# Kernel optimization log

Hardware: AMD Instinct MI355X
Metric: run time of the kernel (lower is better)

The kernel has to match this reference:

```python
import jax, jax.numpy as jnp
import numpy as np

IMAGE_MAX_DIM = 1024.0
POOL_H, POOL_W = 7, 7
LEVEL_THRESH = 48.0


def crop_and_resize(image, boxes, box_idx, crop_h, crop_w):
    """Faithful jax port of tf.image.crop_and_resize (bilinear, extrapolation 0).
    image: [B,H,W,C]; boxes: [N,4] normalized (y1,x1,y2,x2); box_idx: [N] int32.
    Returns [N,crop_h,crop_w,C].
    """
    B, H, W, C = image.shape
    y1, x1, y2, x2 = boxes[:, 0], boxes[:, 1], boxes[:, 2], boxes[:, 3]
    ry = jnp.arange(crop_h, dtype=boxes.dtype) / (crop_h - 1)  # [ph]
    rx = jnp.arange(crop_w, dtype=boxes.dtype) / (crop_w - 1)  # [pw]
    # TF: in_y = y1*(H-1) + i*(y2-y1)*(H-1)/(ph-1)
    ys = (y1[:, None] + ry[None, :] * (y2 - y1)[:, None]) * (H - 1)  # [N,ph]
    xs = (x1[:, None] + rx[None, :] * (x2 - x1)[:, None]) * (W - 1)  # [N,pw]
    y0f = jnp.floor(ys)
    x0f = jnp.floor(xs)
    wy = ys - y0f  # [N,ph]
    wx = xs - x0f  # [N,pw]
    y0 = jnp.clip(y0f, 0, H - 1).astype(jnp.int32)
    yp = jnp.clip(y0f + 1, 0, H - 1).astype(jnp.int32)
    x0 = jnp.clip(x0f, 0, W - 1).astype(jnp.int32)
    xp = jnp.clip(x0f + 1, 0, W - 1).astype(jnp.int32)
    b = box_idx[:, None, None]  # [N,1,1]

    def gather(yy, xx):
        # [N,ph,pw,C] corner gather
        return image[b, yy[:, :, None], xx[:, None, :]]

    wxe = wx[:, None, :, None]  # [N,1,pw,1]
    top = gather(y0, x0) * (1.0 - wxe) + gather(y0, xp) * wxe
    bot = gather(yp, x0) * (1.0 - wxe) + gather(yp, xp) * wxe
    wye = wy[:, :, None, None]  # [N,ph,1,1]
    out = top * (1.0 - wye) + bot * wye
    # extrapolation_value = 0 outside the image
    valid = ((ys >= 0) & (ys <= H - 1))[:, :, None] & ((xs >= 0) & (xs <= W - 1))[:, None, :]
    return jnp.where(valid[..., None], out, jnp.zeros((), dtype=out.dtype))


def setup_inputs() -> dict:
    key = jax.random.key(0)
    k0, k1, k2, k3 = jax.random.split(key, 4)
    B, R, C = 2, 512, 256
    feat0 = jax.random.normal(k0, (B, 256, 256, C), dtype=jnp.float32)
    feat1 = jax.random.normal(k1, (B, 128, 128, C), dtype=jnp.float32)
    # boxes in pixel coords within a 1024x1024 image; sizes 8..128 so both
    # levels (threshold 48 px) are exercised
    tl = jax.random.uniform(k2, (B, R, 2), minval=0.0, maxval=896.0)
    hw = jax.random.uniform(k3, (B, R, 2), minval=8.0, maxval=128.0)
    rois = jnp.concatenate([tl, tl + hw, jnp.zeros((B, R, 1))], axis=-1).astype(jnp.float32)
    return {"feat0": feat0, "feat1": feat1, "rois": rois}


def reference(feat0, feat1, rois):
    B, R = rois.shape[:2]
    C = feat0.shape[-1]
    boxes = rois[..., :4].reshape(B * R, 4)  # pixel coords (y1,x1,y2,x2)
    h = boxes[:, 2] - boxes[:, 0]
    w = boxes[:, 3] - boxes[:, 1]
    # level 1 iff h>48 or w>48 (the scatter_nd of ones), else level 0
    level = (h > LEVEL_THRESH) | (w > LEVEL_THRESH)  # [B*R] bool
    nboxes = jax.lax.stop_gradient(boxes / IMAGE_MAX_DIM)
    box_idx = jnp.repeat(jnp.arange(B, dtype=jnp.int32), R)
    c0 = crop_and_resize(feat0, nboxes, box_idx, POOL_H, POOL_W)
    c1 = crop_and_resize(feat1, nboxes, box_idx, POOL_H, POOL_W)
    # per-box level select replaces the gather/concat/sort/gather reorder chain
    # (which merely restores original (batch, roi) order)
    pooled = jnp.where(level[:, None, None, None], c1, c0)
    return pooled.reshape(B, R, POOL_H, POOL_W, C)
```

## Files before the change

### kernel.cpp

```cpp
#include <hip/hip_runtime.h>


#define POOL 7
#define NCH 256

__global__ __launch_bounds__(256) void roialign_kernel(
    const float* __restrict__ feat0,
    const float* __restrict__ feat1,
    const float* __restrict__ rois,
    float* __restrict__ out,
    int NB, int R)
{
    int t = blockIdx.x * blockDim.x + threadIdx.x;
    int lane = t & 63;
    int wid  = t >> 6;
    int n    = wid / 49;
    if (n >= NB) return;
    int pos  = wid - n * 49;
    int i = pos / POOL;
    int j = pos - i * POOL;

    const float* roi = rois + (size_t)n * 5;
    float y1 = roi[0], x1 = roi[1], y2 = roi[2], x2 = roi[3];

    bool lvl = (y2 - y1 > 48.0f) || (x2 - x1 > 48.0f);
    const float* feat = lvl ? feat1 : feat0;
    int H = lvl ? 128 : 256;
    int W = H;
    int b = n / R;

    const float inv_img = 1.0f / 1024.0f;
    float y1n = y1 * inv_img, y2n = y2 * inv_img;
    float x1n = x1 * inv_img, x2n = x2 * inv_img;

    float ry = (float)i / 6.0f;
    float rx = (float)j / 6.0f;
    float ys = (y1n + ry * (y2n - y1n)) * (float)(H - 1);
    float xs = (x1n + rx * (x2n - x1n)) * (float)(W - 1);

    float y0f = floorf(ys), x0f = floorf(xs);
    float wy = ys - y0f;
    float wx = xs - x0f;

    float Hm1 = (float)(H - 1), Wm1 = (float)(W - 1);
    int y0 = (int)fminf(fmaxf(y0f,        0.0f), Hm1);
    int yp = (int)fminf(fmaxf(y0f + 1.0f, 0.0f), Hm1);
    int x0 = (int)fminf(fmaxf(x0f,        0.0f), Wm1);
    int xp = (int)fminf(fmaxf(x0f + 1.0f, 0.0f), Wm1);

    bool valid = (ys >= 0.0f) && (ys <= Hm1) && (xs >= 0.0f) && (xs <= Wm1);

    size_t plane = (size_t)b * H * W;
    size_t r0 = (plane + (size_t)y0 * W) * NCH;
    size_t r1 = (plane + (size_t)yp * W) * NCH;
    int coff = lane * 4;

    const float4* p00 = (const float4*)(feat + r0 + (size_t)x0 * NCH + coff);
    const float4* p01 = (const float4*)(feat + r0 + (size_t)xp * NCH + coff);
    const float4* p10 = (const float4*)(feat + r1 + (size_t)x0 * NCH + coff);
    const float4* p11 = (const float4*)(feat + r1 + (size_t)xp * NCH + coff);

    float4 v00 = *p00, v01 = *p01, v10 = *p10, v11 = *p11;

    float wx1 = 1.0f - wx, wy1 = 1.0f - wy;
    float4 o;
    {
        float top_x = v00.x * wx1 + v01.x * wx;
        float bot_x = v10.x * wx1 + v11.x * wx;
        o.x = top_x * wy1 + bot_x * wy;
        float top_y = v00.y * wx1 + v01.y * wx;
        float bot_y = v10.y * wx1 + v11.y * wx;
        o.y = top_y * wy1 + bot_y * wy;
        float top_z = v00.z * wx1 + v01.z * wx;
        float bot_z = v10.z * wx1 + v11.z * wx;
        o.z = top_z * wy1 + bot_z * wy;
        float top_w = v00.w * wx1 + v01.w * wx;
        float bot_w = v10.w * wx1 + v11.w * wx;
        o.w = top_w * wy1 + bot_w * wy;
    }
    if (!valid) { o.x = 0.0f; o.y = 0.0f; o.z = 0.0f; o.w = 0.0f; }

    float4* po = (float4*)(out + ((size_t)n * 49 + pos) * NCH + coff);
    *po = o;
}

extern "C" void kernel_launch(void* const* d_in, const int* in_sizes, int n_in,
                              void* d_out, int out_size, void* d_ws, size_t ws_size,
                              hipStream_t stream) {
    const float* feat0 = (const float*)d_in[0];
    const float* feat1 = (const float*)d_in[1];
    const float* rois  = (const float*)d_in[2];
    float* out = (float*)d_out;

    int B  = in_sizes[0] / (256 * 256 * 256);
    int NB = in_sizes[2] / 5;
    int R  = NB / B;

    long long threads = (long long)NB * 49 * 64;
    int block = 256;
    int grid = (int)((threads + block - 1) / block);
    roialign_kernel<<<grid, block, 0, stream>>>(feat0, feat1, rois, out, NB, R);
}
```

Before: 207.4 us.

## Assign one block per ROI with waves looping over pooled bins

```diff
diff --git a/kernel.cpp b/kernel.cpp
--- a/kernel.cpp
+++ b/kernel.cpp
@@ -3,6 +3,8 @@
 
 #define POOL 7
 #define NCH 256
+
+typedef float v4f __attribute__((ext_vector_type(4)));
 
 __global__ __launch_bounds__(256) void roialign_kernel(
     const float* __restrict__ feat0,
@@ -11,14 +13,10 @@
     float* __restrict__ out,
     int NB, int R)
 {
-    int t = blockIdx.x * blockDim.x + threadIdx.x;
-    int lane = t & 63;
-    int wid  = t >> 6;
-    int n    = wid / 49;
+    int n = blockIdx.x;
     if (n >= NB) return;
-    int pos  = wid - n * 49;
-    int i = pos / POOL;
-    int j = pos - i * POOL;
+    int lane = threadIdx.x & 63;
+    int wave = threadIdx.x >> 6;
 
     const float* roi = rois + (size_t)n * 5;
     float y1 = roi[0], x1 = roi[1], y2 = roi[2], x2 = roi[3];
@@ -32,56 +30,47 @@
     const float inv_img = 1.0f / 1024.0f;
     float y1n = y1 * inv_img, y2n = y2 * inv_img;
     float x1n = x1 * inv_img, x2n = x2 * inv_img;
-
-    float ry = (float)i / 6.0f;
-    float rx = (float)j / 6.0f;
-    float ys = (y1n + ry * (y2n - y1n)) * (float)(H - 1);
-    float xs = (x1n + rx * (x2n - x1n)) * (float)(W - 1);
-
-    float y0f = floorf(ys), x0f = floorf(xs);
-    float wy = ys - y0f;
-    float wx = xs - x0f;
-
     float Hm1 = (float)(H - 1), Wm1 = (float)(W - 1);
-    int y0 = (int)fminf(fmaxf(y0f,        0.0f), Hm1);
-    int yp = (int)fminf(fmaxf(y0f + 1.0f, 0.0f), Hm1);
-    int x0 = (int)fminf(fmaxf(x0f,        0.0f), Wm1);
-    int xp = (int)fminf(fmaxf(x0f + 1.0f, 0.0f), Wm1);
-
-    bool valid = (ys >= 0.0f) && (ys <= Hm1) && (xs >= 0.0f) && (xs <= Wm1);
+    float dy = y2n - y1n, dx = x2n - x1n;
 
     size_t plane = (size_t)b * H * W;
-    size_t r0 = (plane + (size_t)y0 * W) * NCH;
-    size_t r1 = (plane + (size_t)yp * W) * NCH;
     int coff = lane * 4;
+    float* outbase = out + (size_t)n * 49 * NCH + coff;
 
-    const float4* p00 = (const float4*)(feat + r0 + (size_t)x0 * NCH + coff);
-    const float4* p01 = (const float4*)(feat + r0 + (size_t)xp * NCH + coff);
-    const float4* p10 = (const float4*)(feat + r1 + (size_t)x0 * NCH + coff);
-    const float4* p11 = (const float4*)(feat + r1 + (size_t)xp * NCH + coff);
+    for (int p = wave; p < 49; p += 4) {
+        int i = p / POOL;
+        int j = p - i * POOL;
 
-    float4 v00 = *p00, v01 = *p01, v10 = *p10, v11 = *p11;
+        float ys = (y1n + ((float)i / 6.0f) * dy) * Hm1;
+        float xs = (x1n + ((float)j / 6.0f) * dx) * Wm1;
 
-    float wx1 = 1.0f - wx, wy1 = 1.0f - wy;
-    float4 o;
-    {
-        float top_x = v00.x * wx1 + v01.x * wx;
-        float bot_x = v10.x * wx1 + v11.x * wx;
-        o.x = top_x * wy1 + bot_x * wy;
-        float top_y = v00.y * wx1 + v01.y * wx;
-        float bot_y = v10.y * wx1 + v11.y * wx;
-        o.y = top_y * wy1 + bot_y * wy;
-        float top_z = v00.z * wx1 + v01.z * wx;
-        float bot_z = v10.z * wx1 + v11.z * wx;
-        o.z = top_z * wy1 + bot_z * wy;
-        float top_w = v00.w * wx1 + v01.w * wx;
-        float bot_w = v10.w * wx1 + v11.w * wx;
-        o.w = top_w * wy1 + bot_w * wy;
+        float y0f = floorf(ys), x0f = floorf(xs);
+        float wy = ys - y0f;
+        float wx = xs - x0f;
+
+        int y0 = (int)fminf(fmaxf(y0f,        0.0f), Hm1);
+        int yp = (int)fminf(fmaxf(y0f + 1.0f, 0.0f), Hm1);
+        int x0 = (int)fminf(fmaxf(x0f,        0.0f), Wm1);
+        int xp = (int)fminf(fmaxf(x0f + 1.0f, 0.0f), Wm1);
+
+        bool valid = (ys >= 0.0f) && (ys <= Hm1) && (xs >= 0.0f) && (xs <= Wm1);
+
+        size_t r0 = (plane + (size_t)y0 * W) * NCH;
+        size_t r1 = (plane + (size_t)yp * W) * NCH;
+
+        v4f v00 = *(const v4f*)(feat + r0 + (size_t)x0 * NCH + coff);
+        v4f v01 = *(const v4f*)(feat + r0 + (size_t)xp * NCH + coff);
+        v4f v10 = *(const v4f*)(feat + r1 + (size_t)x0 * NCH + coff);
+        v4f v11 = *(const v4f*)(feat + r1 + (size_t)xp * NCH + coff);
+
+        float wx1 = 1.0f - wx, wy1 = 1.0f - wy;
+        v4f top = v00 * wx1 + v01 * wx;
+        v4f bot = v10 * wx1 + v11 * wx;
+        v4f o   = top * wy1 + bot * wy;
+        if (!valid) o = (v4f)0.0f;
+
+        *(v4f*)(outbase + (size_t)p * NCH) = o;
     }
-    if (!valid) { o.x = 0.0f; o.y = 0.0f; o.z = 0.0f; o.w = 0.0f; }
-
-    float4* po = (float4*)(out + ((size_t)n * 49 + pos) * NCH + coff);
-    *po = o;
 }
 
 extern "C" void kernel_launch(void* const* d_in, const int* in_sizes, int n_in,
@@ -96,8 +85,5 @@
     int NB = in_sizes[2] / 5;
     int R  = NB / B;
 
-    long long threads = (long long)NB * 49 * 64;
-    int block = 256;
-    int grid = (int)((threads + block - 1) / block);
-    roialign_kernel<<<grid, block, 0, stream>>>(feat0, feat1, rois, out, NB, R);
+    roialign_kernel<<<NB, 256, 0, stream>>>(feat0, feat1, rois, out, NB, R);
 }
```

After: 214.5 us. 3.4% more time.
